# Performance work log

Measured on AMD Instinct MI355X. Metric: run time of the kernel, lower is better.

The kernel has to match this reference:

```python
import jax, jax.numpy as jnp
import numpy as np

K1 = 3                      # spline kernel size per pseudo dim
SIZE = float(np.sqrt(2.0))  # pseudo_cartesian normalization size


def spline_weights(p, k):
    """Degree-1 open B-spline basis over 2D pseudo coords.
    p: [..., 2] in [0,1]. Returns basis [..., 4], weight_index [..., 4]."""
    v = jnp.clip(p, 0.0, 1.0) * (k - 1)
    lo = jnp.floor(v)
    frac = v - lo
    lo = lo.astype(jnp.int32)
    off = jnp.array([0, 1], dtype=jnp.int32)
    w0 = jnp.stack([1.0 - frac[..., 0], frac[..., 0]], axis=-1)   # [...,2]
    w1 = jnp.stack([1.0 - frac[..., 1], frac[..., 1]], axis=-1)   # [...,2]
    i0 = jnp.clip(lo[..., 0:1] + off, 0, k - 1)                    # [...,2]
    i1 = jnp.clip(lo[..., 1:2] + off, 0, k - 1)                    # [...,2]
    basis = (w0[..., :, None] * w1[..., None, :]).reshape(*p.shape[:-1], 4)
    widx = (i0[..., :, None] + k * i1[..., None, :]).reshape(*p.shape[:-1], 4)
    return basis, widx


def setup_inputs() -> dict:
    key = jax.random.key(0)
    kx, ke, kp, kq, kw, kb = jax.random.split(key, 6)
    N, C, P, E, K = 50000, 64, 16, 800000, K1 * K1
    x = jax.random.normal(kx, (N, C), dtype=jnp.float32)
    pos = jax.random.uniform(kp, (N, 2), dtype=jnp.float32)
    pose = jax.random.normal(kq, (N, P, 2), dtype=jnp.float32)
    pose = pose / (jnp.linalg.norm(pose, axis=-1, keepdims=True) + 1e-8)  # unit pose vectors
    W = jax.random.normal(kw, (P, K, C), dtype=jnp.float32) / np.sqrt(C * 4.0)
    bias = jax.random.normal(kb, (P,), dtype=jnp.float32) * 0.01
    edge_index = jax.random.randint(ke, (2, E), 0, N, dtype=jnp.int64)
    return {"x": x, "pos": pos, "pose": pose, "W": W, "bias": bias,
            "edge_index": edge_index}


def reference(x, pos, pose, W, bias, edge_index):
    N, C = x.shape
    P = pose.shape[1]
    row, col = edge_index[0], edge_index[1]
    # pseudo_cartesian: normalized relative position in [0,1]^2
    pseudo = (pos[col] - pos[row]) / (2.0 * SIZE) + 0.5              # [E,2]
    # posevec_to_rotmat on detached pose vectors
    pose_c = jax.lax.stop_gradient(pose)
    a, b = pose_c[..., 0], pose_c[..., 1]
    R = jnp.stack([jnp.stack([a, -b], -1), jnp.stack([b, a], -1)], -2)  # [N,P,2,2]
    Re = R[row]                                                      # [E,P,2,2]
    # rotate pseudo coords about (0.5, 0.5), batched over all poses
    p = jnp.einsum('epij,ej->epi', Re, pseudo - 0.5) + 0.5           # [E,P,2]
    basis, widx = spline_weights(p, K1)                              # [E,P,4]
    # SplineConv (out_channels=1, no root weight, no norm):
    # precompute per-node per-pose per-kernel-bin projections
    Z = jnp.einsum('nc,pkc->npk', x, W)                              # [N,P,K]
    pidx = jnp.arange(P)[None, :, None]
    vals = Z[col[:, None, None], pidx, widx]                         # [E,P,4]
    msg = jnp.sum(basis * vals, axis=-1)                             # [E,P]
    out = jax.ops.segment_sum(msg, row, num_segments=N)              # [N,P]
    return out + bias[None, :]
```

## Files before the change

kernel.cpp:

```cpp
#include <hip/hip_runtime.h>

#define C_DIM 64
#define P_DIM 16
#define K_DIM 9
#define ZROW 10
#define ZNODE (P_DIM * ZROW)
#define INV2S 0.35355339059327373f

typedef __attribute__((ext_vector_type(8))) short short8v;
typedef __attribute__((ext_vector_type(4))) float f32x4;

__device__ __forceinline__ ushort f2bf(float f) {
    uint u = __builtin_bit_cast(uint, f);
    return (ushort)((u + 0x7FFFu + ((u >> 16) & 1u)) >> 16);
}
__device__ __forceinline__ float bf2f(ushort h) {
    return __builtin_bit_cast(float, ((uint)h) << 16);
}

#define ZSTRIDE 72

__global__ __launch_bounds__(256) void z_gemm_kernel(const float* __restrict__ x,
                                                     const float* __restrict__ W,
                                                     const float* __restrict__ bias,
                                                     const float* __restrict__ pose,
                                                     float* __restrict__ out,
                                                     ushort* __restrict__ Zb,
                                                     uint* __restrict__ pose_bf,
                                                     int N) {
    __shared__ ushort w_hi[144 * ZSTRIDE];
    __shared__ ushort w_lo[144 * ZSTRIDE];

    const int tid = threadIdx.x;
    const int block_row = blockIdx.x * 64;

    {
        const float4 b4 = ((const float4*)bias)[tid & 3];
        const int o4 = block_row * 4 + tid;
        if (o4 < N * 4) ((float4*)out)[o4] = b4;
    }

    if (pose_bf != nullptr) {
        for (int i = tid; i < 64 * P_DIM; i += 256) {
            const int r = block_row + (i >> 4);
            if (r < N) {
                const float2 ab = ((const float2*)pose)[(size_t)r * P_DIM + (i & 15)];
                pose_bf[(size_t)r * P_DIM + (i & 15)] =
                    (uint)f2bf(ab.x) | ((uint)f2bf(ab.y) << 16);
            }
        }
    }

    for (int i = tid; i < 144 * (C_DIM / 2); i += 256) {
        const int n  = i >> 5;
        const int k2 = i & 31;
        const float2 w2 = ((const float2*)W)[i];
        const int o = n * ZSTRIDE + k2 * 2;
        const ushort h0 = f2bf(w2.x);
        const ushort h1 = f2bf(w2.y);
        w_hi[o]     = h0;
        w_hi[o + 1] = h1;
        w_lo[o]     = f2bf(w2.x - bf2f(h0));
        w_lo[o + 1] = f2bf(w2.y - bf2f(h1));
    }
    __syncthreads();

    const int lane = tid & 63;
    const int wv   = tid >> 6;
    const int col  = lane & 15;
    const int kg   = lane >> 4;

    const int arow = block_row + wv * 16 + col;
    const float* xr = x + (size_t)(arow < N ? arow : 0) * C_DIM;
    float4 x0 = ((const float4*)xr)[kg * 2];
    float4 x1 = ((const float4*)xr)[kg * 2 + 1];
    float4 x2 = ((const float4*)xr)[8 + kg * 2];
    float4 x3 = ((const float4*)xr)[8 + kg * 2 + 1];
    if (arow >= N) {
        x0 = x1 = x2 = x3 = make_float4(0.f, 0.f, 0.f, 0.f);
    }

    short8v a_hi0, a_lo0, a_hi1, a_lo1;
    {
        const float t0[8] = {x0.x, x0.y, x0.z, x0.w, x1.x, x1.y, x1.z, x1.w};
        const float t1[8] = {x2.x, x2.y, x2.z, x2.w, x3.x, x3.y, x3.z, x3.w};
        #pragma unroll
        for (int e = 0; e < 8; ++e) {
            const ushort h = f2bf(t0[e]);
            a_hi0[e] = (short)h;
            a_lo0[e] = (short)f2bf(t0[e] - bf2f(h));
            const ushort g = f2bf(t1[e]);
            a_hi1[e] = (short)g;
            a_lo1[e] = (short)f2bf(t1[e] - bf2f(g));
        }
    }

    const int orow0 = block_row + wv * 16 + kg * 4;

    #pragma unroll
    for (int nt = 0; nt < 9; ++nt) {
        const ushort* bhp = &w_hi[(nt * 16 + col) * ZSTRIDE + kg * 8];
        const ushort* blp = &w_lo[(nt * 16 + col) * ZSTRIDE + kg * 8];
        const short8v bh0 = *(const short8v*)bhp;
        const short8v bh1 = *(const short8v*)(bhp + 32);
        const short8v bl0 = *(const short8v*)blp;
        const short8v bl1 = *(const short8v*)(blp + 32);

        f32x4 acc = {0.f, 0.f, 0.f, 0.f};
        acc = __builtin_amdgcn_mfma_f32_16x16x32_bf16(a_lo0, bh0, acc, 0, 0, 0);
        acc = __builtin_amdgcn_mfma_f32_16x16x32_bf16(a_hi0, bl0, acc, 0, 0, 0);
        acc = __builtin_amdgcn_mfma_f32_16x16x32_bf16(a_lo1, bh1, acc, 0, 0, 0);
        acc = __builtin_amdgcn_mfma_f32_16x16x32_bf16(a_hi1, bl1, acc, 0, 0, 0);
        acc = __builtin_amdgcn_mfma_f32_16x16x32_bf16(a_hi0, bh0, acc, 0, 0, 0);
        acc = __builtin_amdgcn_mfma_f32_16x16x32_bf16(a_hi1, bh1, acc, 0, 0, 0);

        const int j  = nt * 16 + col;
        const int zi = (j / 9) * ZROW + (j % 9);
        #pragma unroll
        for (int r = 0; r < 4; ++r) {
            const int row = orow0 + r;
            if (row < N) Zb[(size_t)row * ZNODE + zi] = f2bf(acc[r]);
        }
    }
}

#define EILP 8
template <bool USEBF>
__global__ __launch_bounds__(256) void edge_kernel(const int* __restrict__ ei,
                                                   const float* __restrict__ pos,
                                                   const float* __restrict__ pose,
                                                   const uint* __restrict__ pose_bf,
                                                   const ushort* __restrict__ Zb,
                                                   float* __restrict__ out,
                                                   int E) {
    const int p  = threadIdx.x & 15;
    const int eg = threadIdx.x >> 4;
    const int e0 = blockIdx.x * (16 * EILP) + eg;

    int  r[EILP], c[EILP];
    bool valid[EILP];
    #pragma unroll
    for (int it = 0; it < EILP; ++it) {
        int e = e0 + it * 16;
        valid[it] = (e < E);
        int ec = valid[it] ? e : 0;
        r[it] = ei[ec];
        c[it] = ei[E + ec];
    }

    float d0[EILP], d1[EILP];
    #pragma unroll
    for (int it = 0; it < EILP; ++it) {
        const float2 pc = ((const float2*)pos)[c[it]];
        const float2 pr = ((const float2*)pos)[r[it]];
        d0[it] = (pc.x - pr.x) * INV2S;
        d1[it] = (pc.y - pr.y) * INV2S;
    }

    float a_[EILP], b_[EILP];
    #pragma unroll
    for (int it = 0; it < EILP; ++it) {
        if (USEBF) {
            const uint ab = pose_bf[(size_t)r[it] * P_DIM + p];
            a_[it] = bf2f((ushort)(ab & 0xffffu));
            b_[it] = bf2f((ushort)(ab >> 16));
        } else {
            const float2 ab = ((const float2*)pose)[(size_t)r[it] * P_DIM + p];
            a_[it] = ab.x;
            b_[it] = ab.y;
        }
    }

    uint q0[EILP], q1[EILP], q2[EILP], q3[EILP], q4[EILP];
    #pragma unroll
    for (int it = 0; it < EILP; ++it) {
        const uint* Zp = (const uint*)(Zb + (size_t)c[it] * ZNODE) + p * (ZROW / 2);
        q0[it] = Zp[0];
        q1[it] = Zp[1];
        q2[it] = Zp[2];
        q3[it] = Zp[3];
        q4[it] = Zp[4];
    }

    #pragma unroll
    for (int it = 0; it < EILP; ++it) {
        const float p0 = fmaf(a_[it], d0[it], fmaf(-b_[it], d1[it], 0.5f));
        const float p1 = fmaf(b_[it], d0[it], fmaf( a_[it], d1[it], 0.5f));

        const float v0 = fminf(fmaxf(p0, 0.0f), 1.0f) * 2.0f;
        const float v1 = fminf(fmaxf(p1, 0.0f), 1.0f) * 2.0f;
        const bool b0 = (v0 >= 1.0f);
        const bool b1 = (v1 >= 1.0f);
        const float f0 = v0 - (b0 ? 1.0f : 0.0f);
        const float f1 = v1 - (b1 ? 1.0f : 0.0f);

        const uint A0 = q0[it], A1 = q1[it], A2 = q2[it], A3 = q3[it], A4 = q4[it];
        const uint W0 = b1 ? ((A1 >> 16) | (A2 << 16)) : A0;
        const uint W1 = b1 ? ((A2 >> 16) | (A3 << 16)) : A1;
        const uint W2 = b1 ? ((A3 >> 16) | (A4 << 16)) : A2;
        const uint s = b0 ? 16u : 0u;
        const float z00 = bf2f((ushort)(W0 >> s));
        const float z10 = bf2f((ushort)(b0 ? (W1 & 0xffffu) : (W0 >> 16)));
        const float z01 = bf2f((ushort)(b0 ? (W2 & 0xffffu) : (W1 >> 16)));
        const float z11 = bf2f((ushort)(W2 >> s));

        const float w00 = (1.0f - f0) * (1.0f - f1);
        const float w01 = (1.0f - f0) * f1;
        const float w10 = f0 * (1.0f - f1);
        const float w11 = f0 * f1;

        float m = w00 * z00;
        m = fmaf(w01, z01, m);
        m = fmaf(w10, z10, m);
        m = fmaf(w11, z11, m);

        if (valid[it]) atomicAdd(&out[(size_t)r[it] * P_DIM + p], m);
    }
}

extern "C" void kernel_launch(void* const* d_in, const int* in_sizes, int n_in,
                              void* d_out, int out_size, void* d_ws, size_t ws_size,
                              hipStream_t stream) {
    const float* x    = (const float*)d_in[0];
    const float* pos  = (const float*)d_in[1];
    const float* pose = (const float*)d_in[2];
    const float* W    = (const float*)d_in[3];
    const float* bias = (const float*)d_in[4];
    const int*   ei   = (const int*)d_in[5];

    const int N = in_sizes[0] / C_DIM;
    const int E = in_sizes[5] / 2;

    float* out = (float*)d_out;
    ushort* Zb = (ushort*)d_ws;

    const size_t zb_bytes   = (size_t)N * ZNODE * sizeof(ushort);
    const size_t pose_bytes = (size_t)N * P_DIM * sizeof(uint);
    uint* pose_bf = (ws_size >= zb_bytes + pose_bytes)
                        ? (uint*)((char*)d_ws + zb_bytes) : nullptr;

    z_gemm_kernel<<<(N + 63) / 64, 256, 0, stream>>>(x, W, bias, pose, out, Zb, pose_bf, N);

    const int eblocks = (E + 16 * EILP - 1) / (16 * EILP);
    if (pose_bf != nullptr)
        edge_kernel<true><<<eblocks, 256, 0, stream>>>(ei, pos, pose, pose_bf, Zb, out, E);
    else
        edge_kernel<false><<<eblocks, 256, 0, stream>>>(ei, pos, pose, pose_bf, Zb, out, E);
}
```

Baseline: 148.0 us.

## Precompute split-bf16 W once and stage Z tile in LDS for coalesced stores

Result: slower. 156.2 us (+5.6%).

```diff
diff --git a/kernel.cpp b/kernel.cpp
--- a/kernel.cpp
+++ b/kernel.cpp
@@ -5,6 +5,7 @@
 #define K_DIM 9
 #define ZROW 10
 #define ZNODE (P_DIM * ZROW)
+#define WROWS 144
 #define INV2S 0.35355339059327373f
 
 typedef __attribute__((ext_vector_type(8))) short short8v;
@@ -18,18 +19,30 @@
     return __builtin_bit_cast(float, ((uint)h) << 16);
 }
 
-#define ZSTRIDE 72
+__global__ __launch_bounds__(256) void w_prep_kernel(const float* __restrict__ W,
+                                                     ushort* __restrict__ Whi,
+                                                     ushort* __restrict__ Wlo) {
+    const int i = blockIdx.x * 256 + threadIdx.x;
+    if (i < WROWS * (C_DIM / 2)) {
+        const float2 w2 = ((const float2*)W)[i];
+        const ushort h0 = f2bf(w2.x);
+        const ushort h1 = f2bf(w2.y);
+        ((uint*)Whi)[i] = (uint)h0 | ((uint)h1 << 16);
+        ((uint*)Wlo)[i] = (uint)f2bf(w2.x - bf2f(h0)) |
+                          ((uint)f2bf(w2.y - bf2f(h1)) << 16);
+    }
+}
 
 __global__ __launch_bounds__(256) void z_gemm_kernel(const float* __restrict__ x,
-                                                     const float* __restrict__ W,
+                                                     const ushort* __restrict__ Whi,
+                                                     const ushort* __restrict__ Wlo,
                                                      const float* __restrict__ bias,
                                                      const float* __restrict__ pose,
                                                      float* __restrict__ out,
                                                      ushort* __restrict__ Zb,
                                                      uint* __restrict__ pose_bf,
                                                      int N) {
-    __shared__ ushort w_hi[144 * ZSTRIDE];
-    __shared__ ushort w_lo[144 * ZSTRIDE];
+    __shared__ ushort zs[64 * ZNODE];
 
     const int tid = threadIdx.x;
     const int block_row = blockIdx.x * 64;
@@ -50,20 +63,6 @@
             }
         }
     }
-
-    for (int i = tid; i < 144 * (C_DIM / 2); i += 256) {
-        const int n  = i >> 5;
-        const int k2 = i & 31;
-        const float2 w2 = ((const float2*)W)[i];
-        const int o = n * ZSTRIDE + k2 * 2;
-        const ushort h0 = f2bf(w2.x);
-        const ushort h1 = f2bf(w2.y);
-        w_hi[o]     = h0;
-        w_hi[o + 1] = h1;
-        w_lo[o]     = f2bf(w2.x - bf2f(h0));
-        w_lo[o + 1] = f2bf(w2.y - bf2f(h1));
-    }
-    __syncthreads();
 
     const int lane = tid & 63;
     const int wv   = tid >> 6;
@@ -95,16 +94,17 @@
         }
     }
 
-    const int orow0 = block_row + wv * 16 + kg * 4;
+    const int lrow0 = wv * 16 + kg * 4;
 
     #pragma unroll
     for (int nt = 0; nt < 9; ++nt) {
-        const ushort* bhp = &w_hi[(nt * 16 + col) * ZSTRIDE + kg * 8];
-        const ushort* blp = &w_lo[(nt * 16 + col) * ZSTRIDE + kg * 8];
-        const short8v bh0 = *(const short8v*)bhp;
-        const short8v bh1 = *(const short8v*)(bhp + 32);
-        const short8v bl0 = *(const short8v*)blp;
-        const short8v bl1 = *(const short8v*)(blp + 32);
+        const int j = nt * 16 + col;
+        const ushort* bh = Whi + j * C_DIM + kg * 8;
+        const ushort* bl = Wlo + j * C_DIM + kg * 8;
+        const short8v bh0 = *(const short8v*)bh;
+        const short8v bh1 = *(const short8v*)(bh + 32);
+        const short8v bl0 = *(const short8v*)bl;
+        const short8v bl1 = *(const short8v*)(bl + 32);
 
         f32x4 acc = {0.f, 0.f, 0.f, 0.f};
         acc = __builtin_amdgcn_mfma_f32_16x16x32_bf16(a_lo0, bh0, acc, 0, 0, 0);
@@ -114,14 +114,17 @@
         acc = __builtin_amdgcn_mfma_f32_16x16x32_bf16(a_hi0, bh0, acc, 0, 0, 0);
         acc = __builtin_amdgcn_mfma_f32_16x16x32_bf16(a_hi1, bh1, acc, 0, 0, 0);
 
-        const int j  = nt * 16 + col;
         const int zi = (j / 9) * ZROW + (j % 9);
         #pragma unroll
-        for (int r = 0; r < 4; ++r) {
-            const int row = orow0 + r;
-            if (row < N) Zb[(size_t)row * ZNODE + zi] = f2bf(acc[r]);
-        }
-    }
+        for (int r = 0; r < 4; ++r)
+            zs[(lrow0 + r) * ZNODE + zi] = f2bf(acc[r]);
+    }
+    __syncthreads();
+
+    const int nrow = min(64, N - block_row);
+    float4* dst = (float4*)(Zb + (size_t)block_row * ZNODE);
+    for (int i = tid; i < nrow * (ZNODE / 8); i += 256)
+        dst[i] = *(const float4*)&zs[i * 8];
 }
 
 #define EILP 8
@@ -232,14 +235,19 @@
     const int E = in_sizes[5] / 2;
 
     float* out = (float*)d_out;
-    ushort* Zb = (ushort*)d_ws;
-
+
+    ushort* Whi = (ushort*)d_ws;
+    ushort* Wlo = Whi + WROWS * C_DIM;
+    ushort* Zb  = Wlo + WROWS * C_DIM;
+
+    const size_t w_bytes    = (size_t)2 * WROWS * C_DIM * sizeof(ushort);
     const size_t zb_bytes   = (size_t)N * ZNODE * sizeof(ushort);
     const size_t pose_bytes = (size_t)N * P_DIM * sizeof(uint);
-    uint* pose_bf = (ws_size >= zb_bytes + pose_bytes)
-                        ? (uint*)((char*)d_ws + zb_bytes) : nullptr;
-
-    z_gemm_kernel<<<(N + 63) / 64, 256, 0, stream>>>(x, W, bias, pose, out, Zb, pose_bf, N);
+    uint* pose_bf = (ws_size >= w_bytes + zb_bytes + pose_bytes)
+                        ? (uint*)((char*)Zb + zb_bytes) : nullptr;
+
+    w_prep_kernel<<<(WROWS * (C_DIM / 2) + 255) / 256, 256, 0, stream>>>(W, Whi, Wlo);
+    z_gemm_kernel<<<(N + 63) / 64, 256, 0, stream>>>(x, Whi, Wlo, bias, pose, out, Zb, pose_bf, N);
 
     const int eblocks = (E + 16 * EILP - 1) / (16 * EILP);
     if (pose_bf != nullptr)
```

## Pad W to ten bins per pose for contiguous Z stores; drop bf16 pose copy

Applied to the files above, without the earlier changes.

Measured after the change: 153.6 us. 3.8% more time.

```diff
diff --git a/kernel.cpp b/kernel.cpp
--- a/kernel.cpp
+++ b/kernel.cpp
@@ -5,6 +5,7 @@
 #define K_DIM 9
 #define ZROW 10
 #define ZNODE (P_DIM * ZROW)
+#define NT 10
 #define INV2S 0.35355339059327373f
 
 typedef __attribute__((ext_vector_type(8))) short short8v;
@@ -18,18 +19,16 @@
     return __builtin_bit_cast(float, ((uint)h) << 16);
 }
 
-#define ZSTRIDE 72
+#define WSTRIDE 72
 
 __global__ __launch_bounds__(256) void z_gemm_kernel(const float* __restrict__ x,
                                                      const float* __restrict__ W,
                                                      const float* __restrict__ bias,
-                                                     const float* __restrict__ pose,
                                                      float* __restrict__ out,
                                                      ushort* __restrict__ Zb,
-                                                     uint* __restrict__ pose_bf,
                                                      int N) {
-    __shared__ ushort w_hi[144 * ZSTRIDE];
-    __shared__ ushort w_lo[144 * ZSTRIDE];
+    __shared__ ushort w_hi[160 * WSTRIDE];
+    __shared__ ushort w_lo[160 * WSTRIDE];
 
     const int tid = threadIdx.x;
     const int block_row = blockIdx.x * 64;
@@ -40,22 +39,14 @@
         if (o4 < N * 4) ((float4*)out)[o4] = b4;
     }
 
-    if (pose_bf != nullptr) {
-        for (int i = tid; i < 64 * P_DIM; i += 256) {
-            const int r = block_row + (i >> 4);
-            if (r < N) {
-                const float2 ab = ((const float2*)pose)[(size_t)r * P_DIM + (i & 15)];
-                pose_bf[(size_t)r * P_DIM + (i & 15)] =
-                    (uint)f2bf(ab.x) | ((uint)f2bf(ab.y) << 16);
-            }
-        }
-    }
-
-    for (int i = tid; i < 144 * (C_DIM / 2); i += 256) {
-        const int n  = i >> 5;
+    for (int i = tid; i < 160 * (C_DIM / 2); i += 256) {
+        const int s  = i >> 5;
         const int k2 = i & 31;
-        const float2 w2 = ((const float2*)W)[i];
-        const int o = n * ZSTRIDE + k2 * 2;
+        const int p  = s / 10;
+        const int k  = s - p * 10;
+        float2 w2 = make_float2(0.0f, 0.0f);
+        if (k < 9) w2 = ((const float2*)W)[(p * 9 + k) * (C_DIM / 2) + k2];
+        const int o = s * WSTRIDE + k2 * 2;
         const ushort h0 = f2bf(w2.x);
         const ushort h1 = f2bf(w2.y);
         w_hi[o]     = h0;
@@ -98,9 +89,10 @@
     const int orow0 = block_row + wv * 16 + kg * 4;
 
     #pragma unroll
-    for (int nt = 0; nt < 9; ++nt) {
-        const ushort* bhp = &w_hi[(nt * 16 + col) * ZSTRIDE + kg * 8];
-        const ushort* blp = &w_lo[(nt * 16 + col) * ZSTRIDE + kg * 8];
+    for (int nt = 0; nt < NT; ++nt) {
+        const int j = nt * 16 + col;
+        const ushort* bhp = &w_hi[j * WSTRIDE + kg * 8];
+        const ushort* blp = &w_lo[j * WSTRIDE + kg * 8];
         const short8v bh0 = *(const short8v*)bhp;
         const short8v bh1 = *(const short8v*)(bhp + 32);
         const short8v bl0 = *(const short8v*)blp;
@@ -114,22 +106,18 @@
         acc = __builtin_amdgcn_mfma_f32_16x16x32_bf16(a_hi0, bh0, acc, 0, 0, 0);
         acc = __builtin_amdgcn_mfma_f32_16x16x32_bf16(a_hi1, bh1, acc, 0, 0, 0);
 
-        const int j  = nt * 16 + col;
-        const int zi = (j / 9) * ZROW + (j % 9);
         #pragma unroll
         for (int r = 0; r < 4; ++r) {
             const int row = orow0 + r;
-            if (row < N) Zb[(size_t)row * ZNODE + zi] = f2bf(acc[r]);
+            if (row < N) Zb[(size_t)row * ZNODE + j] = f2bf(acc[r]);
         }
     }
 }
 
 #define EILP 8
-template <bool USEBF>
 __global__ __launch_bounds__(256) void edge_kernel(const int* __restrict__ ei,
                                                    const float* __restrict__ pos,
                                                    const float* __restrict__ pose,
-                                                   const uint* __restrict__ pose_bf,
                                                    const ushort* __restrict__ Zb,
                                                    float* __restrict__ out,
                                                    int E) {
@@ -160,15 +148,9 @@
     float a_[EILP], b_[EILP];
     #pragma unroll
     for (int it = 0; it < EILP; ++it) {
-        if (USEBF) {
-            const uint ab = pose_bf[(size_t)r[it] * P_DIM + p];
-            a_[it] = bf2f((ushort)(ab & 0xffffu));
-            b_[it] = bf2f((ushort)(ab >> 16));
-        } else {
-            const float2 ab = ((const float2*)pose)[(size_t)r[it] * P_DIM + p];
-            a_[it] = ab.x;
-            b_[it] = ab.y;
-        }
+        const float2 ab = ((const float2*)pose)[(size_t)r[it] * P_DIM + p];
+        a_[it] = ab.x;
+        b_[it] = ab.y;
     }
 
     uint q0[EILP], q1[EILP], q2[EILP], q3[EILP], q4[EILP];
@@ -234,16 +216,8 @@
     float* out = (float*)d_out;
     ushort* Zb = (ushort*)d_ws;
 
-    const size_t zb_bytes   = (size_t)N * ZNODE * sizeof(ushort);
-    const size_t pose_bytes = (size_t)N * P_DIM * sizeof(uint);
-    uint* pose_bf = (ws_size >= zb_bytes + pose_bytes)
-                        ? (uint*)((char*)d_ws + zb_bytes) : nullptr;
-
-    z_gemm_kernel<<<(N + 63) / 64, 256, 0, stream>>>(x, W, bias, pose, out, Zb, pose_bf, N);
+    z_gemm_kernel<<<(N + 63) / 64, 256, 0, stream>>>(x, W, bias, out, Zb, N);
 
     const int eblocks = (E + 16 * EILP - 1) / (16 * EILP);
-    if (pose_bf != nullptr)
-        edge_kernel<true><<<eblocks, 256, 0, stream>>>(ei, pos, pose, pose_bf, Zb, out, E);
-    else
-        edge_kernel<false><<<eblocks, 256, 0, stream>>>(ei, pos, pose, pose_bf, Zb, out, E);
-}
+    edge_kernel<<<eblocks, 256, 0, stream>>>(ei, pos, pose, Zb, out, E);
+}
```

## Hoist W bf16 split into prep kernel, use padded Z layout and swizzled LDS

Applied to the files above, without the earlier changes.

Result: faster. 144.5 us (median of 2 runs) (-2.3%).

```diff
diff --git a/kernel.cpp b/kernel.cpp
--- a/kernel.cpp
+++ b/kernel.cpp
@@ -5,10 +5,13 @@
 #define K_DIM 9
 #define ZROW 10
 #define ZNODE (P_DIM * ZROW)
+#define NT 10
+#define WELEM (160 * C_DIM)
 #define INV2S 0.35355339059327373f
 
 typedef __attribute__((ext_vector_type(8))) short short8v;
 typedef __attribute__((ext_vector_type(4))) float f32x4;
+typedef uint uint4a __attribute__((ext_vector_type(4), aligned(4)));
 
 __device__ __forceinline__ ushort f2bf(float f) {
     uint u = __builtin_bit_cast(uint, f);
@@ -18,50 +21,64 @@
     return __builtin_bit_cast(float, ((uint)h) << 16);
 }
 
-#define ZSTRIDE 72
+__global__ __launch_bounds__(256) void prep_kernel(const float* __restrict__ W,
+                                                   const float* __restrict__ pose,
+                                                   const float* __restrict__ bias,
+                                                   float* __restrict__ out,
+                                                   ushort* __restrict__ Whi,
+                                                   ushort* __restrict__ Wlo,
+                                                   uint* __restrict__ pose_bf,
+                                                   int N) {
+    const int g = blockIdx.x * 256 + threadIdx.x;
+    const int gsz = gridDim.x * 256;
+
+    if (g < WELEM / 2) {
+        const int j  = g >> 5;
+        const int k2 = g & 31;
+        const int p  = j / 10;
+        const int k  = j - p * 10;
+        float2 w2 = make_float2(0.0f, 0.0f);
+        if (k < 9) w2 = ((const float2*)W)[(p * 9 + k) * (C_DIM / 2) + k2];
+        const ushort h0 = f2bf(w2.x);
+        const ushort h1 = f2bf(w2.y);
+        ((uint*)Whi)[g] = (uint)h0 | ((uint)h1 << 16);
+        ((uint*)Wlo)[g] = (uint)f2bf(w2.x - bf2f(h0)) |
+                          ((uint)f2bf(w2.y - bf2f(h1)) << 16);
+    }
+
+    if (pose_bf != nullptr) {
+        for (int i = g; i < N * P_DIM; i += gsz) {
+            const float2 ab = ((const float2*)pose)[i];
+            pose_bf[i] = (uint)f2bf(ab.x) | ((uint)f2bf(ab.y) << 16);
+        }
+    }
+
+    {
+        const float4 b4 = ((const float4*)bias)[g & 3];
+        for (int i = g; i < N * 4; i += gsz) ((float4*)out)[i] = b4;
+    }
+}
 
 __global__ __launch_bounds__(256) void z_gemm_kernel(const float* __restrict__ x,
-                                                     const float* __restrict__ W,
-                                                     const float* __restrict__ bias,
-                                                     const float* __restrict__ pose,
-                                                     float* __restrict__ out,
+                                                     const ushort* __restrict__ Whi,
+                                                     const ushort* __restrict__ Wlo,
                                                      ushort* __restrict__ Zb,
-                                                     uint* __restrict__ pose_bf,
                                                      int N) {
-    __shared__ ushort w_hi[144 * ZSTRIDE];
-    __shared__ ushort w_lo[144 * ZSTRIDE];
+    __shared__ ushort w_hi[WELEM];
+    __shared__ ushort w_lo[WELEM];
 
     const int tid = threadIdx.x;
     const int block_row = blockIdx.x * 64;
 
-    {
-        const float4 b4 = ((const float4*)bias)[tid & 3];
-        const int o4 = block_row * 4 + tid;
-        if (o4 < N * 4) ((float4*)out)[o4] = b4;
-    }
-
-    if (pose_bf != nullptr) {
-        for (int i = tid; i < 64 * P_DIM; i += 256) {
-            const int r = block_row + (i >> 4);
-            if (r < N) {
-                const float2 ab = ((const float2*)pose)[(size_t)r * P_DIM + (i & 15)];
-                pose_bf[(size_t)r * P_DIM + (i & 15)] =
-                    (uint)f2bf(ab.x) | ((uint)f2bf(ab.y) << 16);
-            }
-        }
-    }
-
-    for (int i = tid; i < 144 * (C_DIM / 2); i += 256) {
-        const int n  = i >> 5;
-        const int k2 = i & 31;
-        const float2 w2 = ((const float2*)W)[i];
-        const int o = n * ZSTRIDE + k2 * 2;
-        const ushort h0 = f2bf(w2.x);
-        const ushort h1 = f2bf(w2.y);
-        w_hi[o]     = h0;
-        w_hi[o + 1] = h1;
-        w_lo[o]     = f2bf(w2.x - bf2f(h0));
-        w_lo[o + 1] = f2bf(w2.y - bf2f(h1));
+    for (int i = tid; i < 160 * 16; i += 256) {
+        const uint4 vh = ((const uint4*)Whi)[i];
+        const uint4 vl = ((const uint4*)Wlo)[i];
+        const int lin = i * 8;
+        const int j   = lin >> 6;
+        const int w   = lin & 63;
+        const int swz = j * 64 + (w ^ ((j & 7) << 3));
+        *(uint4*)&w_hi[swz] = vh;
+        *(uint4*)&w_lo[swz] = vl;
     }
     __syncthreads();
 
@@ -98,13 +115,15 @@
     const int orow0 = block_row + wv * 16 + kg * 4;
 
     #pragma unroll
-    for (int nt = 0; nt < 9; ++nt) {
-        const ushort* bhp = &w_hi[(nt * 16 + col) * ZSTRIDE + kg * 8];
-        const ushort* blp = &w_lo[(nt * 16 + col) * ZSTRIDE + kg * 8];
-        const short8v bh0 = *(const short8v*)bhp;
-        const short8v bh1 = *(const short8v*)(bhp + 32);
-        const short8v bl0 = *(const short8v*)blp;
-        const short8v bl1 = *(const short8v*)(blp + 32);
+    for (int nt = 0; nt < NT; ++nt) {
+        const int j  = nt * 16 + col;
+        const int sx = (j & 7) << 3;
+        const int b0off = j * 64 + ((kg * 8) ^ sx);
+        const int b1off = j * 64 + ((32 + kg * 8) ^ sx);
+        const short8v bh0 = *(const short8v*)&w_hi[b0off];
+        const short8v bh1 = *(const short8v*)&w_hi[b1off];
+        const short8v bl0 = *(const short8v*)&w_lo[b0off];
+        const short8v bl1 = *(const short8v*)&w_lo[b1off];
 
         f32x4 acc = {0.f, 0.f, 0.f, 0.f};
         acc = __builtin_amdgcn_mfma_f32_16x16x32_bf16(a_lo0, bh0, acc, 0, 0, 0);
@@ -114,12 +133,10 @@
         acc = __builtin_amdgcn_mfma_f32_16x16x32_bf16(a_hi0, bh0, acc, 0, 0, 0);
         acc = __builtin_amdgcn_mfma_f32_16x16x32_bf16(a_hi1, bh1, acc, 0, 0, 0);
 
-        const int j  = nt * 16 + col;
-        const int zi = (j / 9) * ZROW + (j % 9);
         #pragma unroll
         for (int r = 0; r < 4; ++r) {
             const int row = orow0 + r;
-            if (row < N) Zb[(size_t)row * ZNODE + zi] = f2bf(acc[r]);
+            if (row < N) Zb[(size_t)row * ZNODE + j] = f2bf(acc[r]);
         }
     }
 }
@@ -171,14 +188,12 @@
         }
     }
 
-    uint q0[EILP], q1[EILP], q2[EILP], q3[EILP], q4[EILP];
+    uint4a qv[EILP];
+    uint   q4[EILP];
     #pragma unroll
     for (int it = 0; it < EILP; ++it) {
         const uint* Zp = (const uint*)(Zb + (size_t)c[it] * ZNODE) + p * (ZROW / 2);
-        q0[it] = Zp[0];
-        q1[it] = Zp[1];
-        q2[it] = Zp[2];
-        q3[it] = Zp[3];
+        qv[it] = *(const uint4a*)Zp;
         q4[it] = Zp[4];
     }
 
@@ -194,7 +209,8 @@
         const float f0 = v0 - (b0 ? 1.0f : 0.0f);
         const float f1 = v1 - (b1 ? 1.0f : 0.0f);
 
-        const uint A0 = q0[it], A1 = q1[it], A2 = q2[it], A3 = q3[it], A4 = q4[it];
+        const uint A0 = qv[it][0], A1 = qv[it][1], A2 = qv[it][2],
+                   A3 = qv[it][3], A4 = q4[it];
         const uint W0 = b1 ? ((A1 >> 16) | (A2 << 16)) : A0;
         const uint W1 = b1 ? ((A2 >> 16) | (A3 << 16)) : A1;
         const uint W2 = b1 ? ((A3 >> 16) | (A4 << 16)) : A2;
@@ -232,14 +248,19 @@
     const int E = in_sizes[5] / 2;
 
     float* out = (float*)d_out;
-    ushort* Zb = (ushort*)d_ws;
-
+
+    ushort* Whi = (ushort*)d_ws;
+    ushort* Wlo = Whi + WELEM;
+    ushort* Zb  = Wlo + WELEM;
+
+    const size_t w_bytes    = (size_t)2 * WELEM * sizeof(ushort);
     const size_t zb_bytes   = (size_t)N * ZNODE * sizeof(ushort);
     const size_t pose_bytes = (size_t)N * P_DIM * sizeof(uint);
-    uint* pose_bf = (ws_size >= zb_bytes + pose_bytes)
-                        ? (uint*)((char*)d_ws + zb_bytes) : nullptr;
-
-    z_gemm_kernel<<<(N + 63) / 64, 256, 0, stream>>>(x, W, bias, pose, out, Zb, pose_bf, N);
+    uint* pose_bf = (ws_size >= w_bytes + zb_bytes + pose_bytes)
+                        ? (uint*)((char*)Zb + zb_bytes) : nullptr;
+
+    prep_kernel<<<3200, 256, 0, stream>>>(W, pose, bias, out, Whi, Wlo, pose_bf, N);
+    z_gemm_kernel<<<(N + 63) / 64, 256, 0, stream>>>(x, Whi, Wlo, Zb, N);
 
     const int eblocks = (E + 16 * EILP - 1) / (16 * EILP);
     if (pose_bf != nullptr)
```
